# Performance work log

Hardware: AMD Instinct MI355X
Metric: run time of the kernel (lower is better)

## Reference

```python
import jax, jax.numpy as jnp
import numpy as np

N, E = 50000, 800000
IN, HID, HEADS, OUT = 128, 64, 2, 32
SLOPE = 0.2  # PyG leaky_relu default


def gat_conv(x, edge_index, edge_attr, W, att_src, att_dst, W_edge, att_edge, bias,
             heads, out_ch, concat):
    n = x.shape[0]
    src, dst = edge_index[0], edge_index[1]
    # add_self_loops with fill_value='mean': self-loop attr = mean of incoming edge_attr
    ones = jnp.ones((src.shape[0],), x.dtype)
    deg = jax.ops.segment_sum(ones, dst, num_segments=n)
    loop_attr = jax.ops.segment_sum(edge_attr, dst, num_segments=n) / jnp.maximum(deg, 1.0)[:, None]
    ar = jnp.arange(n)
    src = jnp.concatenate([src, ar])
    dst = jnp.concatenate([dst, ar])
    ea = jnp.concatenate([edge_attr, loop_attr], axis=0)  # [E+N, 1]
    # linear projections
    h = (x @ W).reshape(n, heads, out_ch)                      # [N,H,C]
    a_src = jnp.sum(h * att_src, axis=-1)                      # [N,H]
    a_dst = jnp.sum(h * att_dst, axis=-1)                      # [N,H]
    e_emb = (ea @ W_edge).reshape(-1, heads, out_ch)           # [E+N,H,C]
    a_edge = jnp.sum(e_emb * att_edge, axis=-1)                # [E+N,H]
    alpha = jax.nn.leaky_relu(a_src[src] + a_dst[dst] + a_edge, SLOPE)
    # segment softmax over destination nodes
    amax = jax.ops.segment_max(alpha, dst, num_segments=n)
    amax = jnp.where(jnp.isfinite(amax), amax, 0.0)
    ex = jnp.exp(alpha - amax[dst])
    denom = jax.ops.segment_sum(ex, dst, num_segments=n)
    coef = ex / (denom[dst] + 1e-16)                           # [E+N,H]
    out = jax.ops.segment_sum(h[src] * coef[:, :, None], dst, num_segments=n)  # [N,H,C]
    out = out.reshape(n, heads * out_ch) if concat else out.mean(axis=1)
    return out + bias


def setup_inputs() -> dict:
    key = jax.random.key(0)
    ks = jax.random.split(key, 16)
    g = lambda k, shape, fan: (jax.random.normal(k, shape, jnp.float32) / np.float32(np.sqrt(fan)))
    x = jax.random.normal(ks[0], (N, IN), jnp.float32)
    edge_index = jax.random.randint(ks[1], (2, E), 0, N)
    edge_weight = jax.random.uniform(ks[2], (E, 1), jnp.float32)
    return dict(
        x=x, edge_index=edge_index, edge_weight=edge_weight,
        W1=g(ks[3], (IN, HEADS * HID), IN),
        att_src1=g(ks[4], (1, HEADS, HID), HID),
        att_dst1=g(ks[5], (1, HEADS, HID), HID),
        We1=g(ks[6], (1, HEADS * HID), 1),
        att_edge1=g(ks[7], (1, HEADS, HID), HID),
        b1=jnp.zeros((HEADS * HID,), jnp.float32),
        W2=g(ks[8], (HEADS * HID, OUT), HEADS * HID),
        att_src2=g(ks[9], (1, 1, OUT), OUT),
        att_dst2=g(ks[10], (1, 1, OUT), OUT),
        We2=g(ks[11], (1, OUT), 1),
        att_edge2=g(ks[12], (1, 1, OUT), OUT),
        b2=jnp.zeros((OUT,), jnp.float32),
    )


def reference(x, edge_index, edge_weight, W1, att_src1, att_dst1, We1, att_edge1, b1,
              W2, att_src2, att_dst2, We2, att_edge2, b2):
    h = gat_conv(x, edge_index, edge_weight, W1, att_src1, att_dst1, We1, att_edge1, b1,
                 HEADS, HID, True)
    h = jax.nn.elu(h)
    out = gat_conv(h, edge_index, edge_weight, W2, att_src2, att_dst2, We2, att_edge2, b2,
                   1, OUT, False)
    return out
```

## Files before the change

### kernel.cpp

```cpp
#include <hip/hip_runtime.h>
#include <hip/hip_bf16.h>
#include <hip/hip_fp16.h>
#include <cstddef>

#define NN 50000
#define EE 800000
#define SB  196
#define EB  3125
#define GB  782

typedef _Float16 half4v __attribute__((ext_vector_type(4)));
typedef _Float16 half8v __attribute__((ext_vector_type(8)));
typedef _Float16 h2v    __attribute__((ext_vector_type(2)));
typedef float    f32x4  __attribute__((ext_vector_type(4)));

__global__ void init_k(unsigned long long* __restrict__ p,
                       const float* __restrict__ We1, const float* __restrict__ attE1,
                       const float* __restrict__ We2, const float* __restrict__ attE2,
                       float* __restrict__ cE) {
    int t = threadIdx.x;
    if (blockIdx.x == SB) {
        __shared__ float smc[128];
        if (t < 128) smc[t] = We1[t] * attE1[t];
        __syncthreads();
        for (int off = 32; off; off >>= 1) {
            if (t < 128 && (t & 63) < off) smc[t] += smc[t + off];
            __syncthreads();
        }
        if (t == 0)  cE[0] = smc[0];
        if (t == 64) cE[1] = smc[64];
        __syncthreads();
        if (t < 32) smc[t] = We2[t] * attE2[t];
        __syncthreads();
        for (int off = 16; off; off >>= 1) {
            if (t < off) smc[t] += smc[t + off];
            __syncthreads();
        }
        if (t == 0) cE[2] = smc[0];
        return;
    }
    int i = blockIdx.x * blockDim.x + t;
    if (i < NN) p[i] = 0ULL;
}

__global__ __launch_bounds__(256) void hist_gemm1_k(
        const int* __restrict__ ei, const float* __restrict__ ew,
        unsigned long long* __restrict__ packed, int* __restrict__ rank,
        const float* __restrict__ x, const float* __restrict__ W,
        const float* __restrict__ attS, const float* __restrict__ attD,
        __half* __restrict__ h1, float* __restrict__ asrc, float* __restrict__ adst) {
    __shared__ __align__(16) _Float16 xs[64 * 136];
    int t = threadIdx.x;
    if (blockIdx.x < EB) {
        int e = blockIdx.x * 256 + t;
        if (e < EE) {
            int dst = ei[EE + e];
            unsigned q = (unsigned)(ew[e] * 16777216.0f + 0.5f);
            unsigned long long old =
                atomicAdd(&packed[dst], (1ULL << 40) | (unsigned long long)q);
            rank[e] = (int)(old >> 40);
        }
        return;
    }
    int rowbase = (blockIdx.x - EB) * 64;
    int wid = t >> 6, lane = t & 63;
    #pragma unroll
    for (int i = 0; i < 8; i++) {
        int idx = t + i * 256;
        int r = idx >> 5;
        int c4 = idx & 31;
        float4 v = make_float4(0.f, 0.f, 0.f, 0.f);
        if (rowbase + r < NN) v = ((const float4*)x)[(size_t)(rowbase + r) * 32 + c4];
        half4v hv = { (_Float16)v.x, (_Float16)v.y, (_Float16)v.z, (_Float16)v.w };
        *(half4v*)&xs[r * 136 + c4 * 4] = hv;
    }
    half8v bf[2][4];
    #pragma unroll
    for (int nt = 0; nt < 2; nt++)
        #pragma unroll
        for (int kk = 0; kk < 4; kk++) {
            int kb = kk * 32 + ((lane >> 4) << 3);
            int c = (wid << 5) + (nt << 4) + (lane & 15);
            half8v f;
            #pragma unroll
            for (int j = 0; j < 8; j++) f[j] = (_Float16)W[(kb + j) * 128 + c];
            bf[nt][kk] = f;
        }
    __syncthreads();
    int ar = lane & 15;
    int ak = (lane >> 4) << 3;
    f32x4 acc[4][2] = {};
    #pragma unroll
    for (int kk = 0; kk < 4; kk++) {
        half8v a[4];
        #pragma unroll
        for (int mt = 0; mt < 4; mt++)
            a[mt] = *(const half8v*)&xs[(mt * 16 + ar) * 136 + kk * 32 + ak];
        #pragma unroll
        for (int mt = 0; mt < 4; mt++)
            #pragma unroll
            for (int nt = 0; nt < 2; nt++)
                acc[mt][nt] = __builtin_amdgcn_mfma_f32_16x16x32_f16(
                    a[mt], bf[nt][kk], acc[mt][nt], 0, 0, 0);
    }
    __syncthreads();
    int drb = (lane >> 4) << 2;
    int dc = (wid << 5) + (lane & 15);
    #pragma unroll
    for (int mt = 0; mt < 4; mt++)
        #pragma unroll
        for (int nt = 0; nt < 2; nt++)
            #pragma unroll
            for (int r = 0; r < 4; r++)
                xs[(mt * 16 + drb + r) * 136 + dc + nt * 16] = (_Float16)acc[mt][nt][r];
    __syncthreads();
    int row = t >> 2;
    int cg = t & 3;
    int grow = rowbase + row;
    float sv = 0.f, dv = 0.f;
    #pragma unroll
    for (int k = 0; k < 4; k++) {
        int c0 = cg * 32 + k * 8;
        half8v hv = *(const half8v*)&xs[row * 136 + c0];
        if (grow < NN) *(half8v*)((_Float16*)h1 + (size_t)grow * 128 + c0) = hv;
        #pragma unroll
        for (int j = 0; j < 8; j++) {
            float f = (float)hv[j];
            sv += f * attS[c0 + j];
            dv += f * attD[c0 + j];
        }
    }
    sv += __shfl_xor(sv, 1);
    dv += __shfl_xor(dv, 1);
    if ((cg & 1) == 0 && grow < NN) {
        asrc[grow * 2 + (cg >> 1)] = sv;
        adst[grow * 2 + (cg >> 1)] = dv;
    }
}

__global__ void loopdiv_k(const unsigned long long* __restrict__ packed,
                          int* __restrict__ deg, float* __restrict__ loopa,
                          int* __restrict__ bsum) {
    __shared__ int sm[256];
    int t = threadIdx.x, n = blockIdx.x * 256 + t;
    int d = 0;
    if (n < NN) {
        unsigned long long p = packed[n];
        d = (int)(p >> 40);
        float ls = (float)(p & ((1ULL << 40) - 1)) * (1.0f / 16777216.0f);
        deg[n] = d;
        loopa[n] = ls / fmaxf((float)d, 1.0f);
    }
    sm[t] = d;
    __syncthreads();
    for (int off = 128; off; off >>= 1) {
        if (t < off) sm[t] += sm[t + off];
        __syncthreads();
    }
    if (!t) bsum[blockIdx.x] = sm[0];
}

__global__ void scan_final_k(const int* __restrict__ deg, const int* __restrict__ bsum,
                             int* __restrict__ rowptr) {
    __shared__ int sm[256];
    __shared__ int boff_s;
    int t = threadIdx.x, b = blockIdx.x, i = b * 256 + t;
    int v0 = (t < b) ? bsum[t] : 0;
    sm[t] = v0;
    __syncthreads();
    for (int off = 128; off; off >>= 1) {
        if (t < off) sm[t] += sm[t + off];
        __syncthreads();
    }
    if (!t) boff_s = sm[0];
    __syncthreads();
    int v = (i < NN) ? deg[i] : 0;
    sm[t] = v;
    __syncthreads();
    for (int off = 1; off < 256; off <<= 1) {
        int a = (t >= off) ? sm[t - off] : 0;
        __syncthreads();
        sm[t] += a;
        __syncthreads();
    }
    if (i < NN) rowptr[i] = boff_s + sm[t] - v;
    if (i == NN - 1) rowptr[NN] = boff_s + sm[t];
}

__global__ void scatter_k(const int* __restrict__ ei, const float* __restrict__ ew,
                          const int* __restrict__ rowptr, const int* __restrict__ rank,
                          int2* __restrict__ csr) {
    int e = blockIdx.x * blockDim.x + threadIdx.x;
    if (e >= EE) return;
    int src = ei[e];
    int dst = ei[EE + e];
    int pos = rowptr[dst] + rank[e];
    csr[pos] = make_int2(src, __float_as_int(ew[e]));
}

__global__ __launch_bounds__(256) void gemm2_k(const __half* __restrict__ z1,
                                               const float* __restrict__ W,
                                               const float* __restrict__ attS,
                                               const float* __restrict__ attD,
                                               __half* __restrict__ h2,
                                               float* __restrict__ asrc,
                                               float* __restrict__ adst) {
    __shared__ __align__(16) _Float16 xs[64 * 136];
    int rowbase = blockIdx.x * 64;
    int t = threadIdx.x;
    int wid = t >> 6, lane = t & 63;
    #pragma unroll
    for (int i = 0; i < 4; i++) {
        int idx = t + i * 256;
        int r = idx >> 4;
        int c16 = idx & 15;
        uint4 v = make_uint4(0, 0, 0, 0);
        if (rowbase + r < NN) v = ((const uint4*)z1)[(size_t)(rowbase + r) * 16 + c16];
        *(uint4*)&xs[r * 136 + c16 * 8] = v;
    }
    half8v bf[2][4];
    #pragma unroll
    for (int nt = 0; nt < 2; nt++)
        #pragma unroll
        for (int kk = 0; kk < 4; kk++) {
            int kb = kk * 32 + ((lane >> 4) << 3);
            int c = (nt << 4) + (lane & 15);
            half8v f;
            #pragma unroll
            for (int j = 0; j < 8; j++) f[j] = (_Float16)W[(kb + j) * 32 + c];
            bf[nt][kk] = f;
        }
    __syncthreads();
    int ar = lane & 15;
    int ak = (lane >> 4) << 3;
    f32x4 acc[2] = {};
    #pragma unroll
    for (int kk = 0; kk < 4; kk++) {
        half8v a = *(const half8v*)&xs[(wid * 16 + ar) * 136 + kk * 32 + ak];
        #pragma unroll
        for (int nt = 0; nt < 2; nt++)
            acc[nt] = __builtin_amdgcn_mfma_f32_16x16x32_f16(a, bf[nt][kk], acc[nt], 0, 0, 0);
    }
    __syncthreads();
    int drb = (lane >> 4) << 2;
    #pragma unroll
    for (int nt = 0; nt < 2; nt++)
        #pragma unroll
        for (int r = 0; r < 4; r++)
            xs[(wid * 16 + drb + r) * 40 + (nt << 4) + (lane & 15)] = (_Float16)acc[nt][r];
    __syncthreads();
    int row = t >> 2;
    int c8 = (t & 3) * 8;
    int grow = rowbase + row;
    half8v hv = *(const half8v*)&xs[row * 40 + c8];
    if (grow < NN) *(half8v*)((_Float16*)h2 + (size_t)grow * 32 + c8) = hv;
    float sv = 0.f, dv = 0.f;
    #pragma unroll
    for (int j = 0; j < 8; j++) {
        float f = (float)hv[j];
        sv += f * attS[c8 + j];
        dv += f * attD[c8 + j];
    }
    sv += __shfl_xor(sv, 1);
    dv += __shfl_xor(dv, 1);
    sv += __shfl_xor(sv, 2);
    dv += __shfl_xor(dv, 2);
    if ((t & 3) == 0 && grow < NN) { asrc[grow] = sv; adst[grow] = dv; }
}

__global__ __launch_bounds__(256) void agg1_k(const int* __restrict__ rowptr,
                       const int2* __restrict__ csr, const float* __restrict__ loopa,
                       const __half* __restrict__ h1, const float* __restrict__ asrc,
                       const float* __restrict__ adst, const float* __restrict__ cE,
                       const float* __restrict__ b1, __half* __restrict__ z1) {
    __shared__ int    ssrc[4][128];
    __shared__ float2 sxx[4][128];
    __shared__ int2   spk[4][136];
    int wid = threadIdx.x >> 6;
    int n = (blockIdx.x * blockDim.x + threadIdx.x) >> 6;
    int lane = threadIdx.x & 63;
    if (n >= NN) return;
    int start = rowptr[n];
    int degn = rowptr[n + 1] - start;
    int total = degn + 1;
    float c0 = cE[0], c1 = cE[1];
    float ad0 = adst[n * 2], ad1 = adst[n * 2 + 1];
    float la = loopa[n];
    float s0 = 0.f, s1 = 0.f;
    for (int i = lane; i < total; i += 64) {
        int src; float w;
        if (i < degn) { int2 sw = csr[start + i]; src = sw.x; w = __int_as_float(sw.y); }
        else          { src = n;                  w = la; }
        float2 as = *(const float2*)&asrc[src * 2];
        float e0 = as.x + ad0 + w * c0; e0 = e0 > 0.f ? e0 : 0.2f * e0;
        float e1 = as.y + ad1 + w * c1; e1 = e1 > 0.f ? e1 : 0.2f * e1;
        float x0 = __expf(e0), x1 = __expf(e1);
        s0 += x0; s1 += x1;
        if (i < 128) { ssrc[wid][i] = src; sxx[wid][i] = make_float2(x0, x1); }
    }
    for (int off = 32; off; off >>= 1) {
        s0 += __shfl_xor(s0, off);
        s1 += __shfl_xor(s1, off);
    }
    float inv0 = 1.0f / (s0 + 1e-16f), inv1 = 1.0f / (s1 + 1e-16f);
    int nst = min(total, 128);
    int nst8 = (nst + 7) & ~7;
    for (int i = lane; i < nst8; i += 64) {
        int2 pk;
        if (i < nst) {
            float2 xv = sxx[wid][i];
            __half2 hh = __floats2half2_rn(xv.x * inv0, xv.y * inv1);
            pk = make_int2(ssrc[wid][i], *(int*)&hh);
        } else pk = make_int2(n, 0);
        spk[wid][i] = pk;
    }
    int hsel = lane >> 5;
    unsigned psel = hsel ? 0x03020302u : 0x01000100u;
    unsigned loff = (unsigned)lane * 4u;
    const char* h1b_ = (const char*)h1;
    float acc0 = 0.f, acc1 = 0.f;
    for (int j = 0; j < nst8; j += 8) {
        h2v pa = {}, pb = {};
        #pragma unroll
        for (int u = 0; u < 8; u++) {
            int2 st = spk[wid][j + u];
            unsigned cs = __builtin_amdgcn_perm(0u, (unsigned)st.y, psel);
            unsigned hb = *(const unsigned*)(h1b_ + (((unsigned)st.x << 8) + loff));
            h2v c; __builtin_memcpy(&c, &cs, 4);
            h2v h; __builtin_memcpy(&h, &hb, 4);
            if (u & 1) pb = c * h + pb;
            else       pa = c * h + pa;
        }
        acc0 += (float)pa.x + (float)pb.x;
        acc1 += (float)pa.y + (float)pb.y;
    }
    for (int base = 128; base < total; base += 64) {
        int i = base + lane;
        float cc0 = 0.f, cc1 = 0.f; int src = n;
        if (i < total) {
            float w;
            if (i < degn) { int2 sw = csr[start + i]; src = sw.x; w = __int_as_float(sw.y); }
            else          { w = la; }
            float e0 = asrc[src * 2]     + ad0 + w * c0; e0 = e0 > 0.f ? e0 : 0.2f * e0;
            float e1 = asrc[src * 2 + 1] + ad1 + w * c1; e1 = e1 > 0.f ? e1 : 0.2f * e1;
            cc0 = __expf(e0) * inv0;
            cc1 = __expf(e1) * inv1;
        }
        int cnt = min(64, total - base);
        for (int jj = 0; jj < cnt; jj++) {
            int   s2 = __shfl(src, jj);
            float k0 = __shfl(cc0, jj);
            float k1 = __shfl(cc1, jj);
            float coef = hsel ? k1 : k0;
            float2 f = __half22float2(*(const __half2*)&h1[(size_t)s2 * 128 + 2 * lane]);
            acc0 += coef * f.x;
            acc1 += coef * f.y;
        }
    }
    float o0 = acc0 + b1[2 * lane];
    float o1 = acc1 + b1[2 * lane + 1];
    o0 = o0 > 0.f ? o0 : expm1f(o0);
    o1 = o1 > 0.f ? o1 : expm1f(o1);
    __half2 oz = __floats2half2_rn(o0, o1);
    *(__half2*)&z1[(size_t)n * 128 + 2 * lane] = oz;
}

__global__ __launch_bounds__(256) void agg2_k(const int* __restrict__ rowptr,
                       const int2* __restrict__ csr, const float* __restrict__ loopa,
                       const __half* __restrict__ hh2, const float* __restrict__ asrc,
                       const float* __restrict__ adst, const float* __restrict__ cE,
                       const float* __restrict__ b2, float* __restrict__ out) {
    __shared__ float2 sxx[4][128];
    __shared__ int    ssrc[4][128];
    __shared__ int2   spk[4][136];
    int wid = threadIdx.x >> 6;
    int n = (blockIdx.x * blockDim.x + threadIdx.x) >> 6;
    int lane = threadIdx.x & 63;
    if (n >= NN) return;
    int start = rowptr[n];
    int degn = rowptr[n + 1] - start;
    int total = degn + 1;
    float c2 = cE[2];
    float aD = adst[n];
    float la = loopa[n];
    float s = 0.f;
    for (int i = lane; i < total; i += 64) {
        int src; float w;
        if (i < degn) { int2 sw = csr[start + i]; src = sw.x; w = __int_as_float(sw.y); }
        else          { src = n;                  w = la; }
        float e = asrc[src] + aD + w * c2;
        e = e > 0.f ? e : 0.2f * e;
        float x = __expf(e);
        s += x;
        if (i < 128) { ssrc[wid][i] = src; sxx[wid][i] = make_float2(x, 0.f); }
    }
    for (int off = 32; off; off >>= 1) s += __shfl_xor(s, off);
    float inv = 1.0f / (s + 1e-16f);
    int nst = min(total, 128);
    int nst8 = (nst + 7) & ~7;
    for (int i = lane; i < nst8; i += 64) {
        int2 pk;
        if (i < nst) {
            float cn = sxx[wid][i].x * inv;
            __half2 hc = __floats2half2_rn(cn, cn);
            pk = make_int2(ssrc[wid][i], *(int*)&hc);
        } else pk = make_int2(n, 0);
        spk[wid][i] = pk;
    }
    int g  = lane >> 4;
    int cp = lane & 15;
    const char* h2b_ = (const char*)hh2;
    unsigned coff = (unsigned)cp * 4u;
    float fa0 = 0.f, fa1 = 0.f;
    h2v pa = {}, pb = {};
    int fold = 0;
    for (int j = 0; j < nst8; j += 8) {
        int2 st0 = spk[wid][j + g];
        int2 st1 = spk[wid][j + 4 + g];
        unsigned hb0 = *(const unsigned*)(h2b_ + (((unsigned)st0.x << 6) + coff));
        unsigned hb1 = *(const unsigned*)(h2b_ + (((unsigned)st1.x << 6) + coff));
        h2v c0v; __builtin_memcpy(&c0v, &st0.y, 4);
        h2v c1v; __builtin_memcpy(&c1v, &st1.y, 4);
        h2v h0; __builtin_memcpy(&h0, &hb0, 4);
        h2v h1v; __builtin_memcpy(&h1v, &hb1, 4);
        pa = c0v * h0 + pa;
        pb = c1v * h1v + pb;
        if (++fold == 4) {
            fa0 += (float)pa.x + (float)pb.x;
            fa1 += (float)pa.y + (float)pb.y;
            pa = {}; pb = {};
            fold = 0;
        }
    }
    fa0 += (float)pa.x + (float)pb.x;
    fa1 += (float)pa.y + (float)pb.y;
    for (int i = 128; i < total; i++) {
        int src; float w;
        if (i < degn) { int2 sw = csr[start + i]; src = sw.x; w = __int_as_float(sw.y); }
        else          { src = n;                  w = la; }
        float e = asrc[src] + aD + w * c2;
        e = e > 0.f ? e : 0.2f * e;
        float cc = __expf(e) * inv;
        if (g == 0) {
            unsigned hb = *(const unsigned*)(h2b_ + (((unsigned)src << 6) + coff));
            h2v h; __builtin_memcpy(&h, &hb, 4);
            fa0 += cc * (float)h.x;
            fa1 += cc * (float)h.y;
        }
    }
    fa0 += __shfl_xor(fa0, 16); fa1 += __shfl_xor(fa1, 16);
    fa0 += __shfl_xor(fa0, 32); fa1 += __shfl_xor(fa1, 32);
    if (lane < 16) {
        float2 o = make_float2(fa0 + b2[2 * cp], fa1 + b2[2 * cp + 1]);
        *(float2*)&out[(size_t)n * 32 + 2 * cp] = o;
    }
}

extern "C" void kernel_launch(void* const* d_in, const int* in_sizes, int n_in,
                              void* d_out, int out_size, void* d_ws, size_t ws_size,
                              hipStream_t stream) {
    const float* x     = (const float*)d_in[0];
    const int*   ei    = (const int*)d_in[1];
    const float* ew    = (const float*)d_in[2];
    const float* W1    = (const float*)d_in[3];
    const float* attS1 = (const float*)d_in[4];
    const float* attD1 = (const float*)d_in[5];
    const float* We1   = (const float*)d_in[6];
    const float* attE1 = (const float*)d_in[7];
    const float* b1    = (const float*)d_in[8];
    const float* W2    = (const float*)d_in[9];
    const float* attS2 = (const float*)d_in[10];
    const float* attD2 = (const float*)d_in[11];
    const float* We2   = (const float*)d_in[12];
    const float* attE2 = (const float*)d_in[13];
    const float* b2    = (const float*)d_in[14];

    char* ws = (char*)d_ws;
    size_t off = 0;
    auto alloc = [&](size_t bytes) -> void* {
        void* p = ws + off;
        off = (off + bytes + 255) & ~(size_t)255;
        return p;
    };
    unsigned long long* packed = (unsigned long long*)alloc((size_t)NN * 8);
    int*    rank    = (int*)alloc((size_t)EE * 4);
    int*    deg     = (int*)alloc((size_t)NN * 4);
    float*  loopa   = (float*)alloc((size_t)NN * 4);
    int*    rowptr  = (int*)alloc((size_t)(NN + 1) * 4);
    int2*   csr     = (int2*)alloc((size_t)EE * 8);
    __half* h1b     = (__half*)alloc((size_t)NN * 128 * 2);
    __half* z1      = (__half*)alloc((size_t)NN * 128 * 2);
    __half* h2b     = (__half*)alloc((size_t)NN * 32 * 2);
    float*  asrc1   = (float*)alloc((size_t)NN * 2 * 4);
    float*  adst1   = (float*)alloc((size_t)NN * 2 * 4);
    float*  asrc2   = (float*)alloc((size_t)NN * 4);
    float*  adst2   = (float*)alloc((size_t)NN * 4);
    float*  cE      = (float*)alloc(4 * 4);
    int*    bsum    = (int*)alloc(256 * 4);

    const int NWB = (NN * 64 + 255) / 256;

    init_k<<<SB + 1, 256, 0, stream>>>(packed, We1, attE1, We2, attE2, cE);
    hist_gemm1_k<<<EB + GB, 256, 0, stream>>>(ei, ew, packed, rank,
                                              x, W1, attS1, attD1, h1b, asrc1, adst1);
    loopdiv_k<<<SB, 256, 0, stream>>>(packed, deg, loopa, bsum);
    scan_final_k<<<SB, 256, 0, stream>>>(deg, bsum, rowptr);
    scatter_k<<<EB, 256, 0, stream>>>(ei, ew, rowptr, rank, csr);

    agg1_k<<<NWB, 256, 0, stream>>>(rowptr, csr, loopa, h1b, asrc1, adst1, cE, b1, z1);
    gemm2_k<<<GB, 256, 0, stream>>>(z1, W2, attS2, attD2, h2b, asrc2, adst2);
    agg2_k<<<NWB, 256, 0, stream>>>(rowptr, csr, loopa, h2b, asrc2, adst2, cE, b2, (float*)d_out);
}
```

Before: 147.8 us.

## Replicate degree histogram across 8 copies and compute self-loop attr in aggregation

Replaces the single packed 64-bit atomic histogram (count plus quantized weight sum) with 8 replicated 32-bit count arrays chosen by block index, which spreads atomic contention. A combine kernel builds per-replica base offsets for the CSR scatter. The self-loop mean attribute is now computed inside the aggregation kernels from the CSR weights, which removes the fixed-point weight accumulation. The GEMM is split from the histogram into its own launch, adding a launch and extra replica memory traffic.

```diff
diff --git a/kernel.cpp b/kernel.cpp
--- a/kernel.cpp
+++ b/kernel.cpp
@@ -8,18 +8,19 @@
 #define SB  196
 #define EB  3125
 #define GB  782
+#define ZB  1563
 
 typedef _Float16 half4v __attribute__((ext_vector_type(4)));
 typedef _Float16 half8v __attribute__((ext_vector_type(8)));
 typedef _Float16 h2v    __attribute__((ext_vector_type(2)));
 typedef float    f32x4  __attribute__((ext_vector_type(4)));
 
-__global__ void init_k(unsigned long long* __restrict__ p,
+__global__ void init_k(unsigned* __restrict__ dreg,
                        const float* __restrict__ We1, const float* __restrict__ attE1,
                        const float* __restrict__ We2, const float* __restrict__ attE2,
                        float* __restrict__ cE) {
     int t = threadIdx.x;
-    if (blockIdx.x == SB) {
+    if (blockIdx.x == ZB) {
         __shared__ float smc[128];
         if (t < 128) smc[t] = We1[t] * attE1[t];
         __syncthreads();
@@ -39,30 +40,94 @@
         if (t == 0) cE[2] = smc[0];
         return;
     }
-    int i = blockIdx.x * blockDim.x + t;
-    if (i < NN) p[i] = 0ULL;
-}
-
-__global__ __launch_bounds__(256) void hist_gemm1_k(
-        const int* __restrict__ ei, const float* __restrict__ ew,
-        unsigned long long* __restrict__ packed, int* __restrict__ rank,
-        const float* __restrict__ x, const float* __restrict__ W,
-        const float* __restrict__ attS, const float* __restrict__ attD,
-        __half* __restrict__ h1, float* __restrict__ asrc, float* __restrict__ adst) {
+    int i = blockIdx.x * 256 + t;
+    if (i < 8 * NN) dreg[i] = 0u;
+}
+
+__global__ void hist_k(const int* __restrict__ ei, unsigned* __restrict__ dreg,
+                       int* __restrict__ rank) {
+    int e = blockIdx.x * 256 + threadIdx.x;
+    if (e >= EE) return;
+    int dst = ei[EE + e];
+    int rep = blockIdx.x & 7;
+    rank[e] = (int)atomicAdd(&dreg[rep * NN + dst], 1u);
+}
+
+__global__ void combine_k(const unsigned* __restrict__ dreg, int* __restrict__ deg,
+                          unsigned short* __restrict__ repbase, int* __restrict__ bsum) {
+    __shared__ int sm[256];
+    int t = threadIdx.x, n = blockIdx.x * 256 + t;
+    int d = 0;
+    if (n < NN) {
+        unsigned base = 0;
+        #pragma unroll
+        for (int r = 0; r < 8; r++) {
+            unsigned c = dreg[r * NN + n];
+            repbase[r * NN + n] = (unsigned short)base;
+            base += c;
+        }
+        d = (int)base;
+        deg[n] = d;
+    }
+    sm[t] = d;
+    __syncthreads();
+    for (int off = 128; off; off >>= 1) {
+        if (t < off) sm[t] += sm[t + off];
+        __syncthreads();
+    }
+    if (!t) bsum[blockIdx.x] = sm[0];
+}
+
+__global__ void scan_final_k(const int* __restrict__ deg, const int* __restrict__ bsum,
+                             int* __restrict__ rowptr) {
+    __shared__ int sm[256];
+    __shared__ int boff_s;
+    int t = threadIdx.x, b = blockIdx.x, i = b * 256 + t;
+    int v0 = (t < b) ? bsum[t] : 0;
+    sm[t] = v0;
+    __syncthreads();
+    for (int off = 128; off; off >>= 1) {
+        if (t < off) sm[t] += sm[t + off];
+        __syncthreads();
+    }
+    if (!t) boff_s = sm[0];
+    __syncthreads();
+    int v = (i < NN) ? deg[i] : 0;
+    sm[t] = v;
+    __syncthreads();
+    for (int off = 1; off < 256; off <<= 1) {
+        int a = (t >= off) ? sm[t - off] : 0;
+        __syncthreads();
+        sm[t] += a;
+        __syncthreads();
+    }
+    if (i < NN) rowptr[i] = boff_s + sm[t] - v;
+    if (i == NN - 1) rowptr[NN] = boff_s + sm[t];
+}
+
+__global__ void scatter_k(const int* __restrict__ ei, const float* __restrict__ ew,
+                          const int* __restrict__ rowptr,
+                          const unsigned short* __restrict__ repbase,
+                          const int* __restrict__ rank, int2* __restrict__ csr) {
+    int e = blockIdx.x * 256 + threadIdx.x;
+    if (e >= EE) return;
+    int src = ei[e];
+    int dst = ei[EE + e];
+    int rep = blockIdx.x & 7;
+    int pos = rowptr[dst] + (int)repbase[rep * NN + dst] + rank[e];
+    csr[pos] = make_int2(src, __float_as_int(ew[e]));
+}
+
+__global__ __launch_bounds__(256) void gemm1_k(const float* __restrict__ x,
+                                               const float* __restrict__ W,
+                                               const float* __restrict__ attS,
+                                               const float* __restrict__ attD,
+                                               __half* __restrict__ h1,
+                                               float* __restrict__ asrc,
+                                               float* __restrict__ adst) {
     __shared__ __align__(16) _Float16 xs[64 * 136];
+    int rowbase = blockIdx.x * 64;
     int t = threadIdx.x;
-    if (blockIdx.x < EB) {
-        int e = blockIdx.x * 256 + t;
-        if (e < EE) {
-            int dst = ei[EE + e];
-            unsigned q = (unsigned)(ew[e] * 16777216.0f + 0.5f);
-            unsigned long long old =
-                atomicAdd(&packed[dst], (1ULL << 40) | (unsigned long long)q);
-            rank[e] = (int)(old >> 40);
-        }
-        return;
-    }
-    int rowbase = (blockIdx.x - EB) * 64;
     int wid = t >> 6, lane = t & 63;
     #pragma unroll
     for (int i = 0; i < 8; i++) {
@@ -136,66 +201,6 @@
         asrc[grow * 2 + (cg >> 1)] = sv;
         adst[grow * 2 + (cg >> 1)] = dv;
     }
-}
-
-__global__ void loopdiv_k(const unsigned long long* __restrict__ packed,
-                          int* __restrict__ deg, float* __restrict__ loopa,
-                          int* __restrict__ bsum) {
-    __shared__ int sm[256];
-    int t = threadIdx.x, n = blockIdx.x * 256 + t;
-    int d = 0;
-    if (n < NN) {
-        unsigned long long p = packed[n];
-        d = (int)(p >> 40);
-        float ls = (float)(p & ((1ULL << 40) - 1)) * (1.0f / 16777216.0f);
-        deg[n] = d;
-        loopa[n] = ls / fmaxf((float)d, 1.0f);
-    }
-    sm[t] = d;
-    __syncthreads();
-    for (int off = 128; off; off >>= 1) {
-        if (t < off) sm[t] += sm[t + off];
-        __syncthreads();
-    }
-    if (!t) bsum[blockIdx.x] = sm[0];
-}
-
-__global__ void scan_final_k(const int* __restrict__ deg, const int* __restrict__ bsum,
-                             int* __restrict__ rowptr) {
-    __shared__ int sm[256];
-    __shared__ int boff_s;
-    int t = threadIdx.x, b = blockIdx.x, i = b * 256 + t;
-    int v0 = (t < b) ? bsum[t] : 0;
-    sm[t] = v0;
-    __syncthreads();
-    for (int off = 128; off; off >>= 1) {
-        if (t < off) sm[t] += sm[t + off];
-        __syncthreads();
-    }
-    if (!t) boff_s = sm[0];
-    __syncthreads();
-    int v = (i < NN) ? deg[i] : 0;
-    sm[t] = v;
-    __syncthreads();
-    for (int off = 1; off < 256; off <<= 1) {
-        int a = (t >= off) ? sm[t - off] : 0;
-        __syncthreads();
-        sm[t] += a;
-        __syncthreads();
-    }
-    if (i < NN) rowptr[i] = boff_s + sm[t] - v;
-    if (i == NN - 1) rowptr[NN] = boff_s + sm[t];
-}
-
-__global__ void scatter_k(const int* __restrict__ ei, const float* __restrict__ ew,
-                          const int* __restrict__ rowptr, const int* __restrict__ rank,
-                          int2* __restrict__ csr) {
-    int e = blockIdx.x * blockDim.x + threadIdx.x;
-    if (e >= EE) return;
-    int src = ei[e];
-    int dst = ei[EE + e];
-    int pos = rowptr[dst] + rank[e];
-    csr[pos] = make_int2(src, __float_as_int(ew[e]));
 }
 
 __global__ __launch_bounds__(256) void gemm2_k(const __half* __restrict__ z1,
@@ -269,7 +274,7 @@
 }
 
 __global__ __launch_bounds__(256) void agg1_k(const int* __restrict__ rowptr,
-                       const int2* __restrict__ csr, const float* __restrict__ loopa,
+                       const int2* __restrict__ csr,
                        const __half* __restrict__ h1, const float* __restrict__ asrc,
                        const float* __restrict__ adst, const float* __restrict__ cE,
                        const float* __restrict__ b1, __half* __restrict__ z1) {
@@ -285,12 +290,12 @@
     int total = degn + 1;
     float c0 = cE[0], c1 = cE[1];
     float ad0 = adst[n * 2], ad1 = adst[n * 2 + 1];
-    float la = loopa[n];
-    float s0 = 0.f, s1 = 0.f;
-    for (int i = lane; i < total; i += 64) {
-        int src; float w;
-        if (i < degn) { int2 sw = csr[start + i]; src = sw.x; w = __int_as_float(sw.y); }
-        else          { src = n;                  w = la; }
+    float s0 = 0.f, s1 = 0.f, sumw = 0.f;
+    for (int i = lane; i < degn; i += 64) {
+        int2 sw = csr[start + i];
+        int src = sw.x;
+        float w = __int_as_float(sw.y);
+        sumw += w;
         float2 as = *(const float2*)&asrc[src * 2];
         float e0 = as.x + ad0 + w * c0; e0 = e0 > 0.f ? e0 : 0.2f * e0;
         float e1 = as.y + ad1 + w * c1; e1 = e1 > 0.f ? e1 : 0.2f * e1;
@@ -301,6 +306,17 @@
     for (int off = 32; off; off >>= 1) {
         s0 += __shfl_xor(s0, off);
         s1 += __shfl_xor(s1, off);
+        sumw += __shfl_xor(sumw, off);
+    }
+    float la = sumw / fmaxf((float)degn, 1.0f);
+    float2 asn = *(const float2*)&asrc[n * 2];
+    float el0 = asn.x + ad0 + la * c0; el0 = el0 > 0.f ? el0 : 0.2f * el0;
+    float el1 = asn.y + ad1 + la * c1; el1 = el1 > 0.f ? el1 : 0.2f * el1;
+    float xl0 = __expf(el0), xl1 = __expf(el1);
+    s0 += xl0; s1 += xl1;
+    if (degn < 128 && lane == (degn & 63)) {
+        ssrc[wid][degn] = n;
+        sxx[wid][degn] = make_float2(xl0, xl1);
     }
     float inv0 = 1.0f / (s0 + 1e-16f), inv1 = 1.0f / (s1 + 1e-16f);
     int nst = min(total, 128);
@@ -366,7 +382,7 @@
 }
 
 __global__ __launch_bounds__(256) void agg2_k(const int* __restrict__ rowptr,
-                       const int2* __restrict__ csr, const float* __restrict__ loopa,
+                       const int2* __restrict__ csr,
                        const __half* __restrict__ hh2, const float* __restrict__ asrc,
                        const float* __restrict__ adst, const float* __restrict__ cE,
                        const float* __restrict__ b2, float* __restrict__ out) {
@@ -382,19 +398,30 @@
     int total = degn + 1;
     float c2 = cE[2];
     float aD = adst[n];
-    float la = loopa[n];
-    float s = 0.f;
-    for (int i = lane; i < total; i += 64) {
-        int src; float w;
-        if (i < degn) { int2 sw = csr[start + i]; src = sw.x; w = __int_as_float(sw.y); }
-        else          { src = n;                  w = la; }
+    float s = 0.f, sumw = 0.f;
+    for (int i = lane; i < degn; i += 64) {
+        int2 sw = csr[start + i];
+        int src = sw.x;
+        float w = __int_as_float(sw.y);
+        sumw += w;
         float e = asrc[src] + aD + w * c2;
         e = e > 0.f ? e : 0.2f * e;
         float x = __expf(e);
         s += x;
         if (i < 128) { ssrc[wid][i] = src; sxx[wid][i] = make_float2(x, 0.f); }
     }
-    for (int off = 32; off; off >>= 1) s += __shfl_xor(s, off);
+    for (int off = 32; off; off >>= 1) {
+        s += __shfl_xor(s, off);
+        sumw += __shfl_xor(sumw, off);
+    }
+    float la = sumw / fmaxf((float)degn, 1.0f);
+    float el = asrc[n] + aD + la * c2; el = el > 0.f ? el : 0.2f * el;
+    float xl = __expf(el);
+    s += xl;
+    if (degn < 128 && lane == (degn & 63)) {
+        ssrc[wid][degn] = n;
+        sxx[wid][degn] = make_float2(xl, 0.f);
+    }
     float inv = 1.0f / (s + 1e-16f);
     int nst = min(total, 128);
     int nst8 = (nst + 7) & ~7;
@@ -482,10 +509,10 @@
         off = (off + bytes + 255) & ~(size_t)255;
         return p;
     };
-    unsigned long long* packed = (unsigned long long*)alloc((size_t)NN * 8);
+    unsigned*       dreg    = (unsigned*)alloc((size_t)NN * 8 * 4);
+    unsigned short* repbase = (unsigned short*)alloc((size_t)NN * 8 * 2);
     int*    rank    = (int*)alloc((size_t)EE * 4);
     int*    deg     = (int*)alloc((size_t)NN * 4);
-    float*  loopa   = (float*)alloc((size_t)NN * 4);
     int*    rowptr  = (int*)alloc((size_t)(NN + 1) * 4);
     int2*   csr     = (int2*)alloc((size_t)EE * 8);
     __half* h1b     = (__half*)alloc((size_t)NN * 128 * 2);
@@ -500,14 +527,15 @@
 
     const int NWB = (NN * 64 + 255) / 256;
 
-    init_k<<<SB + 1, 256, 0, stream>>>(packed, We1, attE1, We2, attE2, cE);
-    hist_gemm1_k<<<EB + GB, 256, 0, stream>>>(ei, ew, packed, rank,
-                                              x, W1, attS1, attD1, h1b, asrc1, adst1);
-    loopdiv_k<<<SB, 256, 0, stream>>>(packed, deg, loopa, bsum);
+    init_k<<<ZB + 1, 256, 0, stream>>>(dreg, We1, attE1, We2, attE2, cE);
+    hist_k<<<EB, 256, 0, stream>>>(ei, dreg, rank);
+    combine_k<<<SB, 256, 0, stream>>>(dreg, deg, repbase, bsum);
     scan_final_k<<<SB, 256, 0, stream>>>(deg, bsum, rowptr);
-    scatter_k<<<EB, 256, 0, stream>>>(ei, ew, rowptr, rank, csr);
-
-    agg1_k<<<NWB, 256, 0, stream>>>(rowptr, csr, loopa, h1b, asrc1, adst1, cE, b1, z1);
+    scatter_k<<<EB, 256, 0, stream>>>(ei, ew, rowptr, repbase, rank, csr);
+
+    gemm1_k<<<GB, 256, 0, stream>>>(x, W1, attS1, attD1, h1b, asrc1, adst1);
+    agg1_k<<<NWB, 256, 0, stream>>>(rowptr, csr, h1b, asrc1, adst1, cE, b1, z1);
+
     gemm2_k<<<GB, 256, 0, stream>>>(z1, W2, attS2, attD2, h2b, asrc2, adst2);
-    agg2_k<<<NWB, 256, 0, stream>>>(rowptr, csr, loopa, h2b, asrc2, adst2, cE, b2, (float*)d_out);
-}
+    agg2_k<<<NWB, 256, 0, stream>>>(rowptr, csr, h2b, asrc2, adst2, cE, b2, (float*)d_out);
+}
```

Result: no change. 147.5 us (-0.1%).
